# Kernel tuning notes

Measured on AMD Instinct MI355X. Metric: run time of the kernel, lower is better.

The kernel has to match this reference:

```python
import jax, jax.numpy as jnp
import numpy as np

B, S, E, H, L, F, V = 8, 1024, 768, 12, 6, 3072, 32000
HD = E // H  # head_dim = 64
EPS = 1e-5


def _pos_encoding(max_len, dim):
    pos = np.arange(max_len, dtype=np.float32)[:, None]
    div = np.exp(np.arange(0, dim, 2, dtype=np.float32) * (-np.log(10000.0) / dim))
    pe = np.zeros((max_len, dim), dtype=np.float32)
    pe[:, 0::2] = np.sin(pos * div)
    pe[:, 1::2] = np.cos(pos * div)
    return jnp.asarray(pe)


def setup_inputs() -> dict:
    key = jax.random.key(0)
    ks = jax.random.split(key, 16)
    sd = 0.02
    inp = {}
    inp['input_ids'] = jax.random.randint(ks[0], (B, S), 0, V)
    inp['attention_mask'] = jnp.ones((B, S), dtype=jnp.int32)
    inp['emb'] = jax.random.normal(ks[1], (V, E), jnp.float32) * sd
    inp['pe'] = _pos_encoding(S, E)
    inp['Wq'] = jax.random.normal(ks[2], (L, E, E), jnp.float32) * sd
    inp['bq'] = jnp.zeros((L, E), jnp.float32)
    inp['Wk'] = jax.random.normal(ks[3], (L, E, E), jnp.float32) * sd
    inp['bk'] = jnp.zeros((L, E), jnp.float32)
    inp['Wv'] = jax.random.normal(ks[4], (L, E, E), jnp.float32) * sd
    inp['bv'] = jnp.zeros((L, E), jnp.float32)
    inp['Wo'] = jax.random.normal(ks[5], (L, E, E), jnp.float32) * sd
    inp['bo'] = jnp.zeros((L, E), jnp.float32)
    inp['ln1_g'] = jnp.ones((L, E), jnp.float32)
    inp['ln1_b'] = jnp.zeros((L, E), jnp.float32)
    inp['W1'] = jax.random.normal(ks[6], (L, E, F), jnp.float32) * sd
    inp['b1'] = jnp.zeros((L, F), jnp.float32)
    inp['W2'] = jax.random.normal(ks[7], (L, F, E), jnp.float32) * sd
    inp['b2'] = jnp.zeros((L, E), jnp.float32)
    inp['ln2_g'] = jnp.ones((L, E), jnp.float32)
    inp['ln2_b'] = jnp.zeros((L, E), jnp.float32)
    inp['Wc'] = jax.random.normal(ks[8], (E, 2), jnp.float32) * sd
    inp['bc'] = jnp.zeros((2,), jnp.float32)
    return inp


def _layernorm(x, g, b):
    mu = jnp.mean(x, axis=-1, keepdims=True)
    var = jnp.mean(jnp.square(x - mu), axis=-1, keepdims=True)
    return (x - mu) * jax.lax.rsqrt(var + EPS) * g + b


def reference(input_ids, attention_mask, emb, pe, Wq, bq, Wk, bk, Wv, bv, Wo, bo,
              ln1_g, ln1_b, W1, b1, W2, b2, ln2_g, ln2_b, Wc, bc):
    x = emb[input_ids] + pe[None, :S, :]           # [B,S,E] (dropout = eval identity)
    mask = attention_mask[:, None, None, :]        # [B,1,1,S]
    scale = jnp.sqrt(jnp.float32(HD))

    def block(x, p):
        wq, bq_, wk, bk_, wv, bv_, wo, bo_, g1, be1, w1, b1_, w2, b2_, g2, be2 = p
        q = (x @ wq + bq_).reshape(B, S, H, HD).transpose(0, 2, 1, 3)  # [B,H,S,D]
        k = (x @ wk + bk_).reshape(B, S, H, HD).transpose(0, 2, 1, 3)
        v = (x @ wv + bv_).reshape(B, S, H, HD).transpose(0, 2, 1, 3)
        scores = jnp.einsum('bhsd,bhtd->bhst', q, k) / scale          # [B,H,S,S]
        scores = jnp.where(mask == 0, -jnp.inf, scores)
        attn = jax.nn.softmax(scores, axis=-1)
        o = jnp.einsum('bhst,bhtd->bhsd', attn, v)
        o = o.transpose(0, 2, 1, 3).reshape(B, S, E) @ wo + bo_
        x = _layernorm(x + o, g1, be1)
        ffn = jax.nn.relu(x @ w1 + b1_) @ w2 + b2_
        x = _layernorm(x + ffn, g2, be2)
        return x, None

    params = (Wq, bq, Wk, bk, Wv, bv, Wo, bo, ln1_g, ln1_b, W1, b1, W2, b2, ln2_g, ln2_b)
    x, _ = jax.lax.scan(block, x, params)
    pooled = jnp.mean(x, axis=1)                   # [B,E]
    return pooled @ Wc + bc                        # [B,2]
```

## Files before the change

### kernel.cpp

```cpp
#include <hip/hip_runtime.h>

typedef __bf16 bf16x8 __attribute__((ext_vector_type(8)));
typedef float  f32x4  __attribute__((ext_vector_type(4)));

constexpr int Bb = 8, Ss = 1024, Ee = 768, Hh = 12, Ll = 6, Ff = 3072;
constexpr int TOK  = Bb * Ss;
constexpr int NQKV = 3 * Ee;

static __device__ __forceinline__ f32x4 mfma16(bf16x8 a, bf16x8 b, f32x4 c) {
  return __builtin_amdgcn_mfma_f32_16x16x32_bf16(a, b, c, 0, 0, 0);
}

static __device__ __forceinline__ void async16(const void* g, void* l) {
  __builtin_amdgcn_global_load_lds(
      (const __attribute__((address_space(1))) unsigned int*)g,
      (__attribute__((address_space(3))) unsigned int*)l, 16, 0, 0);
}

__global__ __launch_bounds__(256) void embed_kernel(
    const int* __restrict__ ids, const float* __restrict__ emb,
    const float* __restrict__ pe, float* __restrict__ x, __bf16* __restrict__ xb)
{
  int tok = blockIdx.x;
  int s   = tok & (Ss - 1);
  int id  = ids[tok];
  const float* er = emb + (size_t)id * Ee;
  const float* pr = pe  + (size_t)s  * Ee;
  size_t base = (size_t)tok * Ee;
#pragma unroll
  for (int i = 0; i < 3; i++) {
    int e = threadIdx.x + i * 256;
    float v = er[e] + pr[e];
    x[base + e]  = v;
    xb[base + e] = (__bf16)v;
  }
}

__global__ __launch_bounds__(256) void transpose_w_kernel(
    const float* __restrict__ src, __bf16* __restrict__ dst,
    int K, int N, size_t sls, size_t dls)
{
  __shared__ float t[32][33];
  src += (size_t)blockIdx.z * sls;
  dst += (size_t)blockIdx.z * dls;
  int n0 = blockIdx.x * 32, k0 = blockIdx.y * 32;
  int c = threadIdx.x & 31, r0 = threadIdx.x >> 5;
#pragma unroll
  for (int rr = 0; rr < 32; rr += 8)
    t[r0 + rr][c] = src[(size_t)(k0 + r0 + rr) * N + n0 + c];
  __syncthreads();
#pragma unroll
  for (int rr = 0; rr < 32; rr += 8)
    dst[(size_t)(n0 + r0 + rr) * K + k0 + c] = (__bf16)t[c][r0 + rr];
}

template<bool OUT_BF16, bool RELU>
__global__ __launch_bounds__(256) void gemm_kernel(
    const __bf16* __restrict__ A, const __bf16* __restrict__ Bt,
    const float* __restrict__ bias0, const float* __restrict__ bias1,
    const float* __restrict__ bias2, int bseg,
    float* __restrict__ Cf, __bf16* __restrict__ Cb, int M, int N, int K)
{
  __shared__ __align__(16) __bf16 lA[128 * 64];
  __shared__ __align__(16) __bf16 lB[128 * 64];
  const int tid  = threadIdx.x;
  const int wave = tid >> 6, lane = tid & 63;
  const int quad = lane >> 4, c16 = lane & 15;
  const int wm = wave >> 1, wn = wave & 1;

  const int bid = blockIdx.x;
  const int xcd = bid & 7;
  const int lb  = bid >> 3;
  const int mb  = xcd * 8 + (lb & 7);
  const int nb  = lb >> 3;
  const size_t m0 = (size_t)mb * 128, n0 = (size_t)nb * 128;

  f32x4 acc[4][4] = {};

  const int srow = tid >> 3;
  const int gcol = ((tid & 7) ^ (srow & 7)) * 8;
  const __bf16* Ag = A  + (m0 + srow) * K + gcol;
  const __bf16* Bg = Bt + (n0 + srow) * K + gcol;

  const int x0 = (quad ^ (c16 & 7)) * 8;
  const int x1 = x0 ^ 32;

  for (int k0 = 0; k0 < K; k0 += 64) {
#pragma unroll
    for (int j = 0; j < 4; j++) {
      async16(Ag + (size_t)(j * 32) * K + k0, lA + ((size_t)tid + j * 256) * 8);
      async16(Bg + (size_t)(j * 32) * K + k0, lB + ((size_t)tid + j * 256) * 8);
    }
    __syncthreads();
    bf16x8 af[4], bfr[4];
#pragma unroll
    for (int mi = 0; mi < 4; mi++)
      af[mi]  = *(const bf16x8*)(lA + (wm * 64 + mi * 16 + c16) * 64 + x0);
#pragma unroll
    for (int ni = 0; ni < 4; ni++)
      bfr[ni] = *(const bf16x8*)(lB + (wn * 64 + ni * 16 + c16) * 64 + x0);
#pragma unroll
    for (int mi = 0; mi < 4; mi++)
#pragma unroll
      for (int ni = 0; ni < 4; ni++)
        acc[mi][ni] = mfma16(af[mi], bfr[ni], acc[mi][ni]);
#pragma unroll
    for (int mi = 0; mi < 4; mi++)
      af[mi]  = *(const bf16x8*)(lA + (wm * 64 + mi * 16 + c16) * 64 + x1);
#pragma unroll
    for (int ni = 0; ni < 4; ni++)
      bfr[ni] = *(const bf16x8*)(lB + (wn * 64 + ni * 16 + c16) * 64 + x1);
#pragma unroll
    for (int mi = 0; mi < 4; mi++)
#pragma unroll
      for (int ni = 0; ni < 4; ni++)
        acc[mi][ni] = mfma16(af[mi], bfr[ni], acc[mi][ni]);
    __syncthreads();
  }

#pragma unroll
  for (int ni = 0; ni < 4; ni++) {
    int col = (int)n0 + wn * 64 + ni * 16 + c16;
    const float* bp = bias0;
    int cc = col;
    if (cc >= bseg) { bp = bias1; cc -= bseg; }
    if (cc >= bseg) { bp = bias2; cc -= bseg; }
    float bv = bp[cc];
#pragma unroll
    for (int mi = 0; mi < 4; mi++) {
#pragma unroll
      for (int rr = 0; rr < 4; rr++) {
        size_t row = m0 + wm * 64 + mi * 16 + quad * 4 + rr;
        float v = acc[mi][ni][rr] + bv;
        if (RELU) v = fmaxf(v, 0.f);
        if (OUT_BF16) Cb[row * N + col] = (__bf16)v;
        else          Cf[row * N + col] = v;
      }
    }
  }
}

__global__ __launch_bounds__(256) void vtrans_kernel(
    const __bf16* __restrict__ qkv, __bf16* __restrict__ vt)
{
  int tid  = blockIdx.x * 256 + threadIdx.x;
  int d    = tid & 63;
  int rest = tid >> 6;
  int sc   = rest & 127;
  int bh   = rest >> 7;
  int b = bh / Hh, h = bh % Hh;
  const __bf16* src = qkv + (size_t)(b * Ss + sc * 8) * NQKV + 2 * Ee + h * 64 + d;
  bf16x8 v;
#pragma unroll
  for (int i = 0; i < 8; i++) v[i] = src[(size_t)i * NQKV];
  *(bf16x8*)(vt + ((size_t)bh * 64 + d) * Ss + sc * 8) = v;
}

__global__ __launch_bounds__(512, 6) void attn_kernel(
    const __bf16* __restrict__ qkv, const __bf16* __restrict__ vt,
    const int* __restrict__ amask, __bf16* __restrict__ out)
{
  __shared__ __align__(16) __bf16 kbuf[2][64 * 64];
  __shared__ __align__(16) __bf16 vbuf[2][64 * 64];
  __shared__ __align__(16) __bf16 plds[8][16 * 68];
  const int idx = blockIdx.x;
  const int bh = idx % 96, qi = idx / 96;
  const int b = bh / Hh, h = bh % Hh;
  const int lane = threadIdx.x & 63, wave = threadIdx.x >> 6;
  const int quad = lane >> 4, c16 = lane & 15;
  const int q0 = qi * 128 + wave * 16;

  const __bf16* qbase = qkv + (size_t)(b * Ss + q0 + c16) * NQKV + h * 64 + quad * 8;
  bf16x8 qf0 = *(const bf16x8*)(qbase);
  bf16x8 qf1 = *(const bf16x8*)(qbase + 32);

  const int srow = threadIdx.x >> 3;
  const int scol = ((threadIdx.x & 7) ^ (srow & 7)) * 8;
  const __bf16* kg = qkv + (size_t)(b * Ss + srow) * NQKV + Ee + h * 64 + scol;
  const __bf16* vg = vt + ((size_t)bh * 64 + srow) * Ss + scol;

  const int sa8 = c16 & 7;
  const int rc0 = (quad ^ sa8) * 8;
  const int rc1 = ((quad + 4) ^ sa8) * 8;

  f32x4 o[4] = {};
  float lrow[4] = {0.f, 0.f, 0.f, 0.f};
  const int* mp = amask + b * Ss;
  __bf16* pw = &plds[wave][0];

  async16(kg, &kbuf[0][(size_t)threadIdx.x * 8]);
  async16(vg, &vbuf[0][(size_t)threadIdx.x * 8]);

  for (int t = 0; t < 16; t++) {
    const int tb = t * 64;
    __syncthreads();
    if (t < 15) {
      const int nb = (t + 1) & 1, ntb = tb + 64;
      async16(kg + (size_t)ntb * NQKV, &kbuf[nb][(size_t)threadIdx.x * 8]);
      async16(vg + ntb,                &vbuf[nb][(size_t)threadIdx.x * 8]);
    }
    const __bf16* kb = &kbuf[t & 1][0];
    const __bf16* vb = &vbuf[t & 1][0];

    f32x4 s[4];
#pragma unroll
    for (int n = 0; n < 4; n++) {
      bf16x8 kf0 = *(const bf16x8*)(kb + (n * 16 + c16) * 64 + rc0);
      bf16x8 kf1 = *(const bf16x8*)(kb + (n * 16 + c16) * 64 + rc1);
      f32x4 z = {};
      z = mfma16(qf0, kf0, z);
      s[n] = mfma16(qf1, kf1, z);
    }
    float mk[4];
#pragma unroll
    for (int n = 0; n < 4; n++) mk[n] = mp[tb + n * 16 + c16] ? 0.f : -1e30f;

#pragma unroll
    for (int rr = 0; rr < 4; rr++) {
      float p0 = __expf(s[0][rr] * 0.125f + mk[0]);
      float p1 = __expf(s[1][rr] * 0.125f + mk[1]);
      float p2 = __expf(s[2][rr] * 0.125f + mk[2]);
      float p3 = __expf(s[3][rr] * 0.125f + mk[3]);
      lrow[rr] += (p0 + p1) + (p2 + p3);
      int prow = (quad * 4 + rr) * 68;
      pw[prow + 0  + c16] = (__bf16)p0;
      pw[prow + 16 + c16] = (__bf16)p1;
      pw[prow + 32 + c16] = (__bf16)p2;
      pw[prow + 48 + c16] = (__bf16)p3;
    }

    bf16x8 pf0 = *(const bf16x8*)(pw + c16 * 68 + quad * 8);
    bf16x8 pf1 = *(const bf16x8*)(pw + c16 * 68 + 32 + quad * 8);
#pragma unroll
    for (int ni = 0; ni < 4; ni++) {
      bf16x8 vf0 = *(const bf16x8*)(vb + (ni * 16 + c16) * 64 + rc0);
      bf16x8 vf1 = *(const bf16x8*)(vb + (ni * 16 + c16) * 64 + rc1);
      o[ni] = mfma16(pf0, vf0, o[ni]);
      o[ni] = mfma16(pf1, vf1, o[ni]);
    }
  }

#pragma unroll
  for (int rr = 0; rr < 4; rr++) {
    float sr = lrow[rr];
    sr += __shfl_xor(sr, 1);
    sr += __shfl_xor(sr, 2);
    sr += __shfl_xor(sr, 4);
    sr += __shfl_xor(sr, 8);
    float inv = 1.f / sr;
    size_t row = (size_t)(b * Ss + q0 + quad * 4 + rr) * Ee + h * 64;
    out[row + 0  + c16] = (__bf16)(o[0][rr] * inv);
    out[row + 16 + c16] = (__bf16)(o[1][rr] * inv);
    out[row + 32 + c16] = (__bf16)(o[2][rr] * inv);
    out[row + 48 + c16] = (__bf16)(o[3][rr] * inv);
  }
}

__global__ __launch_bounds__(256) void add_ln_kernel(
    const float* __restrict__ xin, const float* __restrict__ tmp,
    const float* __restrict__ g, const float* __restrict__ beta,
    float* __restrict__ xout, __bf16* __restrict__ xbout)
{
  __shared__ float red[8];
  size_t base = (size_t)blockIdx.x * Ee;
  float hv[3], s = 0.f, sq = 0.f;
#pragma unroll
  for (int i = 0; i < 3; i++) {
    int e = threadIdx.x + i * 256;
    hv[i] = xin[base + e] + tmp[base + e];
    s += hv[i]; sq += hv[i] * hv[i];
  }
#pragma unroll
  for (int m = 1; m < 64; m <<= 1) { s += __shfl_xor(s, m); sq += __shfl_xor(sq, m); }
  int wave = threadIdx.x >> 6;
  if ((threadIdx.x & 63) == 0) { red[wave] = s; red[4 + wave] = sq; }
  __syncthreads();
  s  = red[0] + red[1] + red[2] + red[3];
  sq = red[4] + red[5] + red[6] + red[7];
  float mean = s * (1.f / Ee);
  float var  = sq * (1.f / Ee) - mean * mean;
  float rstd = rsqrtf(var + 1e-5f);
#pragma unroll
  for (int i = 0; i < 3; i++) {
    int e = threadIdx.x + i * 256;
    float v = (hv[i] - mean) * rstd * g[e] + beta[e];
    xout[base + e]  = v;
    xbout[base + e] = (__bf16)v;
  }
}

__global__ __launch_bounds__(256) void pool1_kernel(
    const float* __restrict__ x, float* __restrict__ partial)
{
  int b = blockIdx.x, chunk = blockIdx.y;
  float acc[3] = {0.f, 0.f, 0.f};
  for (int s = chunk * 64; s < chunk * 64 + 64; s++) {
#pragma unroll
    for (int i = 0; i < 3; i++) {
      int e = threadIdx.x + i * 256;
      acc[i] += x[((size_t)b * Ss + s) * Ee + e];
    }
  }
#pragma unroll
  for (int i = 0; i < 3; i++) {
    int e = threadIdx.x + i * 256;
    partial[((size_t)b * 16 + chunk) * Ee + e] = acc[i];
  }
}

__global__ __launch_bounds__(256) void pool2_kernel(
    const float* __restrict__ partial, const float* __restrict__ Wc,
    const float* __restrict__ bc, float* __restrict__ out)
{
  __shared__ float red[8];
  int b = blockIdx.x;
  float p0 = 0.f, p1 = 0.f;
#pragma unroll
  for (int i = 0; i < 3; i++) {
    int e = threadIdx.x + i * 256;
    float pe_ = 0.f;
#pragma unroll
    for (int c = 0; c < 16; c++) pe_ += partial[((size_t)b * 16 + c) * Ee + e];
    pe_ *= (1.f / Ss);
    p0 += pe_ * Wc[e * 2 + 0];
    p1 += pe_ * Wc[e * 2 + 1];
  }
#pragma unroll
  for (int m = 1; m < 64; m <<= 1) { p0 += __shfl_xor(p0, m); p1 += __shfl_xor(p1, m); }
  int wave = threadIdx.x >> 6;
  if ((threadIdx.x & 63) == 0) { red[wave] = p0; red[4 + wave] = p1; }
  __syncthreads();
  if (threadIdx.x == 0) {
    out[b * 2 + 0] = red[0] + red[1] + red[2] + red[3] + bc[0];
    out[b * 2 + 1] = red[4] + red[5] + red[6] + red[7] + bc[1];
  }
}

extern "C" void kernel_launch(void* const* d_in, const int* in_sizes, int n_in,
                              void* d_out, int out_size, void* d_ws, size_t ws_size,
                              hipStream_t stream) {
  const int*   ids   = (const int*)  d_in[0];
  const int*   amask = (const int*)  d_in[1];
  const float* emb   = (const float*)d_in[2];
  const float* pe    = (const float*)d_in[3];
  const float* Wq    = (const float*)d_in[4];
  const float* bq    = (const float*)d_in[5];
  const float* Wk    = (const float*)d_in[6];
  const float* bk    = (const float*)d_in[7];
  const float* Wv    = (const float*)d_in[8];
  const float* bv    = (const float*)d_in[9];
  const float* Wo    = (const float*)d_in[10];
  const float* bo    = (const float*)d_in[11];
  const float* ln1g  = (const float*)d_in[12];
  const float* ln1b  = (const float*)d_in[13];
  const float* W1    = (const float*)d_in[14];
  const float* b1    = (const float*)d_in[15];
  const float* W2    = (const float*)d_in[16];
  const float* b2    = (const float*)d_in[17];
  const float* ln2g  = (const float*)d_in[18];
  const float* ln2b  = (const float*)d_in[19];
  const float* Wc    = (const float*)d_in[20];
  const float* bc    = (const float*)d_in[21];
  float* outp = (float*)d_out;

  char* p = (char*)d_ws;
  auto alloc = [&](size_t bytes) { char* r = p; p += (bytes + 255) & ~(size_t)255; return r; };
  float*  x     = (float*) alloc((size_t)TOK * Ee * 4);
  __bf16* xb    = (__bf16*)alloc((size_t)TOK * Ee * 2);
  float*  tmp   = (float*) alloc((size_t)TOK * Ee * 4);
  __bf16* attn  = (__bf16*)alloc((size_t)TOK * Ee * 2);
  char*   r1    = alloc((size_t)TOK * Ff * 2);
  __bf16* qkv   = (__bf16*)r1;
  __bf16* vt    = (__bf16*)(r1 + (size_t)TOK * NQKV * 2);
  __bf16* h1    = (__bf16*)r1;
  __bf16* wqkvt = (__bf16*)alloc((size_t)Ll * NQKV * Ee * 2);
  __bf16* wot   = (__bf16*)alloc((size_t)Ll * Ee * Ee * 2);
  __bf16* w1t   = (__bf16*)alloc((size_t)Ll * Ff * Ee * 2);
  __bf16* w2t   = (__bf16*)alloc((size_t)Ll * Ee * Ff * 2);
  float*  part  = (float*) alloc((size_t)Bb * 16 * Ee * 4);

  embed_kernel<<<TOK, 256, 0, stream>>>(ids, emb, pe, x, xb);

  transpose_w_kernel<<<dim3(Ee/32, Ee/32, Ll), 256, 0, stream>>>(
      Wq, wqkvt,                         Ee, Ee, (size_t)Ee*Ee, (size_t)NQKV*Ee);
  transpose_w_kernel<<<dim3(Ee/32, Ee/32, Ll), 256, 0, stream>>>(
      Wk, wqkvt + (size_t)Ee*Ee,         Ee, Ee, (size_t)Ee*Ee, (size_t)NQKV*Ee);
  transpose_w_kernel<<<dim3(Ee/32, Ee/32, Ll), 256, 0, stream>>>(
      Wv, wqkvt + (size_t)2*Ee*Ee,       Ee, Ee, (size_t)Ee*Ee, (size_t)NQKV*Ee);
  transpose_w_kernel<<<dim3(Ee/32, Ee/32, Ll), 256, 0, stream>>>(
      Wo, wot,                           Ee, Ee, (size_t)Ee*Ee, (size_t)Ee*Ee);
  transpose_w_kernel<<<dim3(Ff/32, Ee/32, Ll), 256, 0, stream>>>(
      W1, w1t,                           Ee, Ff, (size_t)Ee*Ff, (size_t)Ff*Ee);
  transpose_w_kernel<<<dim3(Ee/32, Ff/32, Ll), 256, 0, stream>>>(
      W2, w2t,                           Ff, Ee, (size_t)Ff*Ee, (size_t)Ee*Ff);

  for (int l = 0; l < Ll; l++) {
    gemm_kernel<true, false><<<64 * (NQKV/128), 256, 0, stream>>>(
        xb, wqkvt + (size_t)l*NQKV*Ee,
        bq + l*Ee, bk + l*Ee, bv + l*Ee, Ee,
        nullptr, qkv, TOK, NQKV, Ee);
    vtrans_kernel<<<3072, 256, 0, stream>>>(qkv, vt);
    attn_kernel<<<768, 512, 0, stream>>>(qkv, vt, amask, attn);
    gemm_kernel<false, false><<<64 * (Ee/128), 256, 0, stream>>>(
        attn, wot + (size_t)l*Ee*Ee,
        bo + l*Ee, bo + l*Ee, bo + l*Ee, Ee,
        tmp, nullptr, TOK, Ee, Ee);
    add_ln_kernel<<<TOK, 256, 0, stream>>>(x, tmp, ln1g + l*Ee, ln1b + l*Ee, x, xb);
    gemm_kernel<true, true><<<64 * (Ff/128), 256, 0, stream>>>(
        xb, w1t + (size_t)l*Ff*Ee,
        b1 + l*Ff, b1 + l*Ff, b1 + l*Ff, Ff,
        nullptr, h1, TOK, Ff, Ee);
    gemm_kernel<false, false><<<64 * (Ee/128), 256, 0, stream>>>(
        h1, w2t + (size_t)l*Ee*Ff,
        b2 + l*Ee, b2 + l*Ee, b2 + l*Ee, Ee,
        tmp, nullptr, TOK, Ee, Ff);
    add_ln_kernel<<<TOK, 256, 0, stream>>>(x, tmp, ln2g + l*Ee, ln2b + l*Ee, x, xb);
  }

  pool1_kernel<<<dim3(Bb, 16), 256, 0, stream>>>(x, part);
  pool2_kernel<<<Bb, 256, 0, stream>>>(part, Wc, bc, outp);
}
```

Measured before the change: 2.138 ms.

## Double-buffer LDS tiles in GEMM kernel to overlap loads with MFMA

```diff
diff --git a/kernel.cpp b/kernel.cpp
--- a/kernel.cpp
+++ b/kernel.cpp
@@ -61,8 +61,8 @@
     const float* __restrict__ bias2, int bseg,
     float* __restrict__ Cf, __bf16* __restrict__ Cb, int M, int N, int K)
 {
-  __shared__ __align__(16) __bf16 lA[128 * 64];
-  __shared__ __align__(16) __bf16 lB[128 * 64];
+  __shared__ __align__(16) __bf16 lA[2][128 * 64];
+  __shared__ __align__(16) __bf16 lB[2][128 * 64];
   const int tid  = threadIdx.x;
   const int wave = tid >> 6, lane = tid & 63;
   const int quad = lane >> 4, c16 = lane & 15;
@@ -85,20 +85,34 @@
   const int x0 = (quad ^ (c16 & 7)) * 8;
   const int x1 = x0 ^ 32;
 
-  for (int k0 = 0; k0 < K; k0 += 64) {
-#pragma unroll
-    for (int j = 0; j < 4; j++) {
-      async16(Ag + (size_t)(j * 32) * K + k0, lA + ((size_t)tid + j * 256) * 8);
-      async16(Bg + (size_t)(j * 32) * K + k0, lB + ((size_t)tid + j * 256) * 8);
-    }
-    __syncthreads();
+  const int nk = K >> 6;
+
+#pragma unroll
+  for (int j = 0; j < 4; j++) {
+    async16(Ag + (size_t)(j * 32) * K, &lA[0][((size_t)tid + j * 256) * 8]);
+    async16(Bg + (size_t)(j * 32) * K, &lB[0][((size_t)tid + j * 256) * 8]);
+  }
+  __syncthreads();
+
+  for (int kt = 0; kt < nk; ++kt) {
+    const int cur = kt & 1;
+    if (kt + 1 < nk) {
+      const int k1 = (kt + 1) << 6;
+#pragma unroll
+      for (int j = 0; j < 4; j++) {
+        async16(Ag + (size_t)(j * 32) * K + k1, &lA[cur ^ 1][((size_t)tid + j * 256) * 8]);
+        async16(Bg + (size_t)(j * 32) * K + k1, &lB[cur ^ 1][((size_t)tid + j * 256) * 8]);
+      }
+    }
+    const __bf16* la = &lA[cur][0];
+    const __bf16* lb = &lB[cur][0];
     bf16x8 af[4], bfr[4];
 #pragma unroll
     for (int mi = 0; mi < 4; mi++)
-      af[mi]  = *(const bf16x8*)(lA + (wm * 64 + mi * 16 + c16) * 64 + x0);
+      af[mi]  = *(const bf16x8*)(la + (wm * 64 + mi * 16 + c16) * 64 + x0);
 #pragma unroll
     for (int ni = 0; ni < 4; ni++)
-      bfr[ni] = *(const bf16x8*)(lB + (wn * 64 + ni * 16 + c16) * 64 + x0);
+      bfr[ni] = *(const bf16x8*)(lb + (wn * 64 + ni * 16 + c16) * 64 + x0);
 #pragma unroll
     for (int mi = 0; mi < 4; mi++)
 #pragma unroll
@@ -106,10 +120,10 @@
         acc[mi][ni] = mfma16(af[mi], bfr[ni], acc[mi][ni]);
 #pragma unroll
     for (int mi = 0; mi < 4; mi++)
-      af[mi]  = *(const bf16x8*)(lA + (wm * 64 + mi * 16 + c16) * 64 + x1);
+      af[mi]  = *(const bf16x8*)(la + (wm * 64 + mi * 16 + c16) * 64 + x1);
 #pragma unroll
     for (int ni = 0; ni < 4; ni++)
-      bfr[ni] = *(const bf16x8*)(lB + (wn * 64 + ni * 16 + c16) * 64 + x1);
+      bfr[ni] = *(const bf16x8*)(lb + (wn * 64 + ni * 16 + c16) * 64 + x1);
 #pragma unroll
     for (int mi = 0; mi < 4; mi++)
 #pragma unroll
```

Measured after the change: 2.063 ms. 3.5% less time.

## Triple-buffer GEMM LDS tiles with K=32 stages and async prefetch pipeline

Applied to the files above, without the earlier changes.

```diff
diff --git a/kernel.cpp b/kernel.cpp
--- a/kernel.cpp
+++ b/kernel.cpp
@@ -55,14 +55,14 @@
 }
 
 template<bool OUT_BF16, bool RELU>
-__global__ __launch_bounds__(256) void gemm_kernel(
+__global__ __launch_bounds__(256, 3) void gemm_kernel(
     const __bf16* __restrict__ A, const __bf16* __restrict__ Bt,
     const float* __restrict__ bias0, const float* __restrict__ bias1,
     const float* __restrict__ bias2, int bseg,
     float* __restrict__ Cf, __bf16* __restrict__ Cb, int M, int N, int K)
 {
-  __shared__ __align__(16) __bf16 lA[128 * 64];
-  __shared__ __align__(16) __bf16 lB[128 * 64];
+  __shared__ __align__(16) __bf16 lA[3][64 * 64];
+  __shared__ __align__(16) __bf16 lB[3][64 * 64];
   const int tid  = threadIdx.x;
   const int wave = tid >> 6, lane = tid & 63;
   const int quad = lane >> 4, c16 = lane & 15;
@@ -77,45 +77,74 @@
 
   f32x4 acc[4][4] = {};
 
-  const int srow = tid >> 3;
-  const int gcol = ((tid & 7) ^ (srow & 7)) * 8;
-  const __bf16* Ag = A  + (m0 + srow) * K + gcol;
-  const __bf16* Bg = Bt + (n0 + srow) * K + gcol;
-
-  const int x0 = (quad ^ (c16 & 7)) * 8;
-  const int x1 = x0 ^ 32;
-
-  for (int k0 = 0; k0 < K; k0 += 64) {
-#pragma unroll
-    for (int j = 0; j < 4; j++) {
-      async16(Ag + (size_t)(j * 32) * K + k0, lA + ((size_t)tid + j * 256) * 8);
-      async16(Bg + (size_t)(j * 32) * K + k0, lB + ((size_t)tid + j * 256) * 8);
-    }
-    __syncthreads();
+  const int s0l = tid >> 3;
+  const int s0c = tid & 7;
+  const int l0  = s0c ^ (s0l & 7);
+  const int tr0 = (s0l << 1) | (l0 >> 2);
+  const int gc0 = (l0 & 3) * 8;
+  const int s1l = (tid + 256) >> 3;
+  const int l1  = s0c ^ (s1l & 7);
+  const int tr1 = (s1l << 1) | (l1 >> 2);
+  const int gc1 = (l1 & 3) * 8;
+
+  const __bf16* Ag0 = A  + (m0 + tr0) * K + gc0;
+  const __bf16* Ag1 = A  + (m0 + tr1) * K + gc1;
+  const __bf16* Bg0 = Bt + (n0 + tr0) * K + gc0;
+  const __bf16* Bg1 = Bt + (n0 + tr1) * K + gc1;
+  const int d0 = tid * 8;
+
+  const int nk = K >> 5;
+
+  auto stage = [&](int t, int slot) {
+    const int kof = t << 5;
+    async16(Ag0 + kof, &lA[slot][d0]);
+    async16(Ag1 + kof, &lA[slot][d0 + 2048]);
+    async16(Bg0 + kof, &lB[slot][d0]);
+    async16(Bg1 + kof, &lB[slot][d0 + 2048]);
+  };
+
+  int aoff[4], boff[4];
+#pragma unroll
+  for (int f = 0; f < 4; f++) {
+    int ra = wm * 64 + f * 16 + c16;
+    int ja = ra >> 1;
+    aoff[f] = ja * 64 + (((((ra & 1) << 2) | quad)) ^ (ja & 7)) * 8;
+    int rb = wn * 64 + f * 16 + c16;
+    int jb = rb >> 1;
+    boff[f] = jb * 64 + (((((rb & 1) << 2) | quad)) ^ (jb & 7)) * 8;
+  }
+
+  stage(0, 0);
+  stage(1, 1);
+  asm volatile("s_waitcnt vmcnt(4)" ::: "memory");
+  __builtin_amdgcn_s_barrier();
+  __builtin_amdgcn_sched_barrier(0);
+
+  int slot = 0;
+  for (int t = 0; t < nk; ++t) {
+    if (t + 2 < nk) {
+      int ns = slot + 2; if (ns >= 3) ns -= 3;
+      stage(t + 2, ns);
+    }
+    const __bf16* la = &lA[slot][0];
+    const __bf16* lb = &lB[slot][0];
     bf16x8 af[4], bfr[4];
 #pragma unroll
-    for (int mi = 0; mi < 4; mi++)
-      af[mi]  = *(const bf16x8*)(lA + (wm * 64 + mi * 16 + c16) * 64 + x0);
-#pragma unroll
-    for (int ni = 0; ni < 4; ni++)
-      bfr[ni] = *(const bf16x8*)(lB + (wn * 64 + ni * 16 + c16) * 64 + x0);
+    for (int f = 0; f < 4; f++) af[f]  = *(const bf16x8*)(la + aoff[f]);
+#pragma unroll
+    for (int f = 0; f < 4; f++) bfr[f] = *(const bf16x8*)(lb + boff[f]);
+    __builtin_amdgcn_s_setprio(1);
 #pragma unroll
     for (int mi = 0; mi < 4; mi++)
 #pragma unroll
       for (int ni = 0; ni < 4; ni++)
         acc[mi][ni] = mfma16(af[mi], bfr[ni], acc[mi][ni]);
-#pragma unroll
-    for (int mi = 0; mi < 4; mi++)
-      af[mi]  = *(const bf16x8*)(lA + (wm * 64 + mi * 16 + c16) * 64 + x1);
-#pragma unroll
-    for (int ni = 0; ni < 4; ni++)
-      bfr[ni] = *(const bf16x8*)(lB + (wn * 64 + ni * 16 + c16) * 64 + x1);
-#pragma unroll
-    for (int mi = 0; mi < 4; mi++)
-#pragma unroll
-      for (int ni = 0; ni < 4; ni++)
-        acc[mi][ni] = mfma16(af[mi], bfr[ni], acc[mi][ni]);
-    __syncthreads();
+    __builtin_amdgcn_s_setprio(0);
+    if (t + 2 < nk) asm volatile("s_waitcnt vmcnt(4)" ::: "memory");
+    else            asm volatile("s_waitcnt vmcnt(0)" ::: "memory");
+    __builtin_amdgcn_s_barrier();
+    __builtin_amdgcn_sched_barrier(0);
+    slot = (slot + 1 == 3) ? 0 : slot + 1;
   }
 
 #pragma unroll
```

Result: faster. 2.064 ms (-3.5%).

## Double-buffer GEMM B tiles, load A directly to registers, split-K narrow GEMMs

Applied to the files above, without the earlier changes.

```diff
diff --git a/kernel.cpp b/kernel.cpp
--- a/kernel.cpp
+++ b/kernel.cpp
@@ -55,14 +55,14 @@
 }
 
 template<bool OUT_BF16, bool RELU>
-__global__ __launch_bounds__(256) void gemm_kernel(
+__global__ __launch_bounds__(256, 3) void gemm_kernel(
     const __bf16* __restrict__ A, const __bf16* __restrict__ Bt,
     const float* __restrict__ bias0, const float* __restrict__ bias1,
     const float* __restrict__ bias2, int bseg,
-    float* __restrict__ Cf, __bf16* __restrict__ Cb, int M, int N, int K)
-{
-  __shared__ __align__(16) __bf16 lA[128 * 64];
-  __shared__ __align__(16) __bf16 lB[128 * 64];
+    float* __restrict__ Cf, __bf16* __restrict__ Cb, int M, int N, int K,
+    int nbt, int ks, size_t cstride)
+{
+  __shared__ __align__(16) __bf16 lB[2][128 * 64];
   const int tid  = threadIdx.x;
   const int wave = tid >> 6, lane = tid & 63;
   const int quad = lane >> 4, c16 = lane & 15;
@@ -72,52 +72,112 @@
   const int xcd = bid & 7;
   const int lb  = bid >> 3;
   const int mb  = xcd * 8 + (lb & 7);
-  const int nb  = lb >> 3;
+  const int sup = lb >> 3;
+  const int nb  = sup % nbt;
+  const int sp  = sup / nbt;
   const size_t m0 = (size_t)mb * 128, n0 = (size_t)nb * 128;
+
+  const int kn   = K / ks;
+  const int kbeg = sp * kn;
+  const int nk   = kn >> 6;
 
   f32x4 acc[4][4] = {};
 
   const int srow = tid >> 3;
   const int gcol = ((tid & 7) ^ (srow & 7)) * 8;
-  const __bf16* Ag = A  + (m0 + srow) * K + gcol;
-  const __bf16* Bg = Bt + (n0 + srow) * K + gcol;
-
+  const __bf16* Bg = Bt + (n0 + srow) * K + kbeg + gcol;
   const int x0 = (quad ^ (c16 & 7)) * 8;
   const int x1 = x0 ^ 32;
 
-  for (int k0 = 0; k0 < K; k0 += 64) {
-#pragma unroll
-    for (int j = 0; j < 4; j++) {
-      async16(Ag + (size_t)(j * 32) * K + k0, lA + ((size_t)tid + j * 256) * 8);
-      async16(Bg + (size_t)(j * 32) * K + k0, lB + ((size_t)tid + j * 256) * 8);
+  const __bf16* Aw = A + (m0 + wm * 64 + c16) * (size_t)K + kbeg + quad * 8;
+  const size_t arow = (size_t)16 * K;
+
+  bf16x8 afP[4], afQ[4], af1[4], bfr[4];
+
+#pragma unroll
+  for (int j = 0; j < 4; j++)
+    async16(Bg + (size_t)(j * 32) * K, &lB[0][((size_t)tid + j * 256) * 8]);
+#pragma unroll
+  for (int mi = 0; mi < 4; mi++)
+    afP[mi] = *(const bf16x8*)(Aw + mi * arow);
+  __syncthreads();
+
+  for (int t = 0; t < nk; t += 2) {
+#pragma unroll
+    for (int j = 0; j < 4; j++)
+      async16(Bg + (size_t)(j * 32) * K + (t + 1) * 64,
+              &lB[1][((size_t)tid + j * 256) * 8]);
+#pragma unroll
+    for (int mi = 0; mi < 4; mi++)
+      afQ[mi] = *(const bf16x8*)(Aw + mi * arow + (t + 1) * 64);
+#pragma unroll
+    for (int mi = 0; mi < 4; mi++)
+      af1[mi] = *(const bf16x8*)(Aw + mi * arow + t * 64 + 32);
+    {
+      const __bf16* lb0 = &lB[0][0];
+#pragma unroll
+      for (int ni = 0; ni < 4; ni++)
+        bfr[ni] = *(const bf16x8*)(lb0 + (wn * 64 + ni * 16 + c16) * 64 + x0);
+      __builtin_amdgcn_s_setprio(1);
+#pragma unroll
+      for (int mi = 0; mi < 4; mi++)
+#pragma unroll
+        for (int ni = 0; ni < 4; ni++)
+          acc[mi][ni] = mfma16(afP[mi], bfr[ni], acc[mi][ni]);
+      __builtin_amdgcn_s_setprio(0);
+#pragma unroll
+      for (int ni = 0; ni < 4; ni++)
+        bfr[ni] = *(const bf16x8*)(lb0 + (wn * 64 + ni * 16 + c16) * 64 + x1);
+      __builtin_amdgcn_s_setprio(1);
+#pragma unroll
+      for (int mi = 0; mi < 4; mi++)
+#pragma unroll
+        for (int ni = 0; ni < 4; ni++)
+          acc[mi][ni] = mfma16(af1[mi], bfr[ni], acc[mi][ni]);
+      __builtin_amdgcn_s_setprio(0);
     }
     __syncthreads();
-    bf16x8 af[4], bfr[4];
+
+    if (t + 2 < nk) {
+#pragma unroll
+      for (int j = 0; j < 4; j++)
+        async16(Bg + (size_t)(j * 32) * K + (t + 2) * 64,
+                &lB[0][((size_t)tid + j * 256) * 8]);
+#pragma unroll
+      for (int mi = 0; mi < 4; mi++)
+        afP[mi] = *(const bf16x8*)(Aw + mi * arow + (t + 2) * 64);
+    }
 #pragma unroll
     for (int mi = 0; mi < 4; mi++)
-      af[mi]  = *(const bf16x8*)(lA + (wm * 64 + mi * 16 + c16) * 64 + x0);
-#pragma unroll
-    for (int ni = 0; ni < 4; ni++)
-      bfr[ni] = *(const bf16x8*)(lB + (wn * 64 + ni * 16 + c16) * 64 + x0);
-#pragma unroll
-    for (int mi = 0; mi < 4; mi++)
+      af1[mi] = *(const bf16x8*)(Aw + mi * arow + (t + 1) * 64 + 32);
+    {
+      const __bf16* lb1 = &lB[1][0];
 #pragma unroll
       for (int ni = 0; ni < 4; ni++)
-        acc[mi][ni] = mfma16(af[mi], bfr[ni], acc[mi][ni]);
-#pragma unroll
-    for (int mi = 0; mi < 4; mi++)
-      af[mi]  = *(const bf16x8*)(lA + (wm * 64 + mi * 16 + c16) * 64 + x1);
-#pragma unroll
-    for (int ni = 0; ni < 4; ni++)
-      bfr[ni] = *(const bf16x8*)(lB + (wn * 64 + ni * 16 + c16) * 64 + x1);
-#pragma unroll
-    for (int mi = 0; mi < 4; mi++)
+        bfr[ni] = *(const bf16x8*)(lb1 + (wn * 64 + ni * 16 + c16) * 64 + x0);
+      __builtin_amdgcn_s_setprio(1);
+#pragma unroll
+      for (int mi = 0; mi < 4; mi++)
+#pragma unroll
+        for (int ni = 0; ni < 4; ni++)
+          acc[mi][ni] = mfma16(afQ[mi], bfr[ni], acc[mi][ni]);
+      __builtin_amdgcn_s_setprio(0);
 #pragma unroll
       for (int ni = 0; ni < 4; ni++)
-        acc[mi][ni] = mfma16(af[mi], bfr[ni], acc[mi][ni]);
+        bfr[ni] = *(const bf16x8*)(lb1 + (wn * 64 + ni * 16 + c16) * 64 + x1);
+      __builtin_amdgcn_s_setprio(1);
+#pragma unroll
+      for (int mi = 0; mi < 4; mi++)
+#pragma unroll
+        for (int ni = 0; ni < 4; ni++)
+          acc[mi][ni] = mfma16(af1[mi], bfr[ni], acc[mi][ni]);
+      __builtin_amdgcn_s_setprio(0);
+    }
     __syncthreads();
   }
 
+  float* Cfs = Cf + (size_t)sp * cstride;
+  const bool addb = (sp == 0);
 #pragma unroll
   for (int ni = 0; ni < 4; ni++) {
     int col = (int)n0 + wn * 64 + ni * 16 + c16;
@@ -125,7 +185,7 @@
     int cc = col;
     if (cc >= bseg) { bp = bias1; cc -= bseg; }
     if (cc >= bseg) { bp = bias2; cc -= bseg; }
-    float bv = bp[cc];
+    float bv = addb ? bp[cc] : 0.f;
 #pragma unroll
     for (int mi = 0; mi < 4; mi++) {
 #pragma unroll
@@ -134,7 +194,7 @@
         float v = acc[mi][ni][rr] + bv;
         if (RELU) v = fmaxf(v, 0.f);
         if (OUT_BF16) Cb[row * N + col] = (__bf16)v;
-        else          Cf[row * N + col] = v;
+        else          Cfs[row * N + col] = v;
       }
     }
   }
@@ -257,7 +317,8 @@
 }
 
 __global__ __launch_bounds__(256) void add_ln_kernel(
-    const float* __restrict__ xin, const float* __restrict__ tmp,
+    const float* __restrict__ xin, const float* __restrict__ t0,
+    const float* __restrict__ t1,
     const float* __restrict__ g, const float* __restrict__ beta,
     float* __restrict__ xout, __bf16* __restrict__ xbout)
 {
@@ -267,7 +328,7 @@
 #pragma unroll
   for (int i = 0; i < 3; i++) {
     int e = threadIdx.x + i * 256;
-    hv[i] = xin[base + e] + tmp[base + e];
+    hv[i] = xin[base + e] + t0[base + e] + t1[base + e];
     s += hv[i]; sq += hv[i] * hv[i];
   }
 #pragma unroll
@@ -368,6 +429,7 @@
   float*  x     = (float*) alloc((size_t)TOK * Ee * 4);
   __bf16* xb    = (__bf16*)alloc((size_t)TOK * Ee * 2);
   float*  tmp   = (float*) alloc((size_t)TOK * Ee * 4);
+  float*  tmp2  = (float*) alloc((size_t)TOK * Ee * 4);
   __bf16* attn  = (__bf16*)alloc((size_t)TOK * Ee * 2);
   char*   r1    = alloc((size_t)TOK * Ff * 2);
   __bf16* qkv   = (__bf16*)r1;
@@ -378,6 +440,8 @@
   __bf16* w1t   = (__bf16*)alloc((size_t)Ll * Ff * Ee * 2);
   __bf16* w2t   = (__bf16*)alloc((size_t)Ll * Ee * Ff * 2);
   float*  part  = (float*) alloc((size_t)Bb * 16 * Ee * 4);
+
+  const size_t CSTR = (size_t)TOK * Ee;
 
   embed_kernel<<<TOK, 256, 0, stream>>>(ids, emb, pe, x, xb);
 
@@ -398,23 +462,23 @@
     gemm_kernel<true, false><<<64 * (NQKV/128), 256, 0, stream>>>(
         xb, wqkvt + (size_t)l*NQKV*Ee,
         bq + l*Ee, bk + l*Ee, bv + l*Ee, Ee,
-        nullptr, qkv, TOK, NQKV, Ee);
+        nullptr, qkv, TOK, NQKV, Ee, NQKV/128, 1, 0);
     vtrans_kernel<<<3072, 256, 0, stream>>>(qkv, vt);
     attn_kernel<<<768, 512, 0, stream>>>(qkv, vt, amask, attn);
-    gemm_kernel<false, false><<<64 * (Ee/128), 256, 0, stream>>>(
+    gemm_kernel<false, false><<<64 * (Ee/128) * 2, 256, 0, stream>>>(
         attn, wot + (size_t)l*Ee*Ee,
         bo + l*Ee, bo + l*Ee, bo + l*Ee, Ee,
-        tmp, nullptr, TOK, Ee, Ee);
-    add_ln_kernel<<<TOK, 256, 0, stream>>>(x, tmp, ln1g + l*Ee, ln1b + l*Ee, x, xb);
+        tmp, nullptr, TOK, Ee, Ee, Ee/128, 2, CSTR);
+    add_ln_kernel<<<TOK, 256, 0, stream>>>(x, tmp, tmp2, ln1g + l*Ee, ln1b + l*Ee, x, xb);
     gemm_kernel<true, true><<<64 * (Ff/128), 256, 0, stream>>>(
         xb, w1t + (size_t)l*Ff*Ee,
         b1 + l*Ff, b1 + l*Ff, b1 + l*Ff, Ff,
-        nullptr, h1, TOK, Ff, Ee);
-    gemm_kernel<false, false><<<64 * (Ee/128), 256, 0, stream>>>(
+        nullptr, h1, TOK, Ff, Ee, Ff/128, 1, 0);
+    gemm_kernel<false, false><<<64 * (Ee/128) * 2, 256, 0, stream>>>(
         h1, w2t + (size_t)l*Ee*Ff,
         b2 + l*Ee, b2 + l*Ee, b2 + l*Ee, Ee,
-        tmp, nullptr, TOK, Ee, Ff);
-    add_ln_kernel<<<TOK, 256, 0, stream>>>(x, tmp, ln2g + l*Ee, ln2b + l*Ee, x, xb);
+        tmp, nullptr, TOK, Ee, Ff, Ee/128, 2, CSTR);
+    add_ln_kernel<<<TOK, 256, 0, stream>>>(x, tmp, tmp2, ln2g + l*Ee, ln2b + l*Ee, x, xb);
   }
 
   pool1_kernel<<<dim3(Bb, 16), 256, 0, stream>>>(x, part);
```

Measured after the change: 2.861 ms. +33.8%, slower.
